# Performance work log

Measured on AMD Instinct MI355X. Metric: run time of the kernel, lower is better.

The kernel has to match this reference:

```python
import jax, jax.numpy as jnp
import numpy as np

B, CI, CO = 2, 32, 32
NX, NY, NZ = 64, 64, 64
M1, M2, M3 = 8, 8, 8
ZH = NZ // 2 + 1


def _dft_mat(N, sign):
    # Dense DFT twiddle matrix W[k, n] = exp(sign * 2j*pi*k*n/N), complex64.
    a = jnp.arange(N)
    ph = (sign * 2.0) * jnp.pi * jnp.outer(a, a).astype(jnp.float32) / N
    return jnp.exp(1j * ph)


def setup_inputs() -> dict:
    key = jax.random.key(0)
    ks = jax.random.split(key, 9)
    scale = 1.0 / (CI * CO)
    x = jax.random.normal(ks[0], (B, CI, NX, NY, NZ), dtype=jnp.float32)
    wshape = (CI, CO, M1, M2, M3)
    names = ['w1r', 'w1i', 'w2r', 'w2i', 'w3r', 'w3i', 'w4r', 'w4i']
    out = {'x': x}
    for i, nm in enumerate(names):
        out[nm] = scale * jax.random.uniform(ks[i + 1], wshape, dtype=jnp.float32)
    return out


def _dht3(x):
    # Naive O(N^2)-per-axis 3D DFT via dense matmuls; return real part.
    Wx = _dft_mat(NX, -1)
    Wy = _dft_mat(NY, -1)
    Wz = _dft_mat(NZ, -1)
    y = x.astype(jnp.complex64)
    y = jnp.einsum('bcxyz,xa->bcayz', y, Wx)
    y = jnp.einsum('bcxyz,ya->bcxaz', y, Wy)
    y = jnp.einsum('bcxyz,za->bcxya', y, Wz)
    return y.real


def _idht3(X):
    # Inverse DFT via dense matmuls; rectangular (ZH -> NZ) on last axis.
    Wxi = _dft_mat(NX, +1) / NX
    Wyi = _dft_mat(NY, +1) / NY
    kz = jnp.arange(ZH)
    nz = jnp.arange(NZ)
    Wzi = jnp.exp(1j * (2.0 * jnp.pi * jnp.outer(kz, nz).astype(jnp.float32) / NZ)) / NZ
    y = jnp.einsum('bcxyz,xa->bcayz', X, Wxi)
    y = jnp.einsum('bcxyz,ya->bcxaz', y, Wyi)
    y = jnp.einsum('bcxyz,za->bcxya', y, Wzi)
    return y.real


def _mul(a, b):
    # compl_mul3d: contract over input channels in the mode block.
    return jnp.einsum('bixyz,ioxyz->boxyz', a, b)


def reference(x, w1r, w1i, w2r, w2i, w3r, w3i, w4r, w4i):
    w1 = w1r + 1j * w1i
    w2 = w2r + 1j * w2i
    w3 = w3r + 1j * w3i
    w4 = w4r + 1j * w4i

    xd = _dht3(x)  # [B, CI, NX, NY, NZ] real

    out = jnp.zeros((B, CO, NX, NY, ZH), dtype=jnp.complex64)
    out = out.at[:, :, :M1, :M2, :M3].set(_mul(xd[:, :, :M1, :M2, :M3], w1))
    out = out.at[:, :, NX - M1:, :M2, :M3].set(_mul(xd[:, :, NX - M1:, :M2, :M3], w2))
    out = out.at[:, :, :M1, NY - M2:, :M3].set(_mul(xd[:, :, :M1, NY - M2:, :M3], w3))
    out = out.at[:, :, NX - M1:, NY - M2:, :M3].set(_mul(xd[:, :, NX - M1:, NY - M2:, :M3], w4))

    return _idht3(out)  # [B, CO, NX, NY, NZ] real
```

## Files before the change

### kernel.cpp

```cpp
#include <hip/hip_runtime.h>

#define PI2_64 0.098174770424681038f


__global__ __launch_bounds__(256) void k_fwd_z(const float* __restrict__ x,
                                               float* __restrict__ z1) {
  __shared__ __align__(16) float lx[256 * 65];
  __shared__ float czs[64], szs[64];
  int tid = threadIdx.x;
  long base = (long)blockIdx.x * (256 * 64);
  const float4* xg = (const float4*)(x + base);
#pragma unroll
  for (int j = 0; j < 16; ++j) {
    int idx = j * 256 + tid;
    float4 v = xg[idx];
    int flat = idx << 2;
    int r = flat >> 6, c = flat & 63;
    float* dst = &lx[r * 65 + c];
    dst[0] = v.x; dst[1] = v.y; dst[2] = v.z; dst[3] = v.w;
  }
  if (tid < 64) {
    float s, c;
    __sincosf(-PI2_64 * (float)tid, &s, &c);
    czs[tid] = c; szs[tid] = s;
  }
  __syncthreads();

  float ar[8] = {0,0,0,0,0,0,0,0}, ai[8] = {0,0,0,0,0,0,0,0};
  const float* row = &lx[tid * 65];
  for (int z = 0; z < 64; ++z) {
    float xv = row[z];
    float bc = czs[z], bs = szs[z];
    float wr = 1.f, wi = 0.f;
#pragma unroll
    for (int k = 0; k < 8; ++k) {
      ar[k] = fmaf(xv, wr, ar[k]);
      ai[k] = fmaf(xv, wi, ai[k]);
      float nr = wr * bc - wi * bs;
      wi = wr * bs + wi * bc;
      wr = nr;
    }
  }
  float4* o = (float4*)(z1 + ((long)blockIdx.x * 256 + tid) * 16);
  o[0] = make_float4(ar[0], ai[0], ar[1], ai[1]);
  o[1] = make_float4(ar[2], ai[2], ar[3], ai[3]);
  o[2] = make_float4(ar[4], ai[4], ar[5], ai[5]);
  o[3] = make_float4(ar[6], ai[6], ar[7], ai[7]);
}

__global__ __launch_bounds__(128) void k_fwd_y(const float* __restrict__ z1,
                                               float* __restrict__ z2) {
  __shared__ __align__(16) float s[64 * 16];
  int tid = threadIdx.x;
  const float4* src = (const float4*)(z1 + (long)blockIdx.x * 1024);
  float4* l4 = (float4*)s;
  l4[tid] = src[tid];
  l4[tid + 128] = src[tid + 128];
  __syncthreads();
  int ky = tid >> 3, kz = tid & 7;
  int f = (ky < 8) ? ky : 48 + ky;
  float bs, bc; __sincosf(-PI2_64 * (float)f, &bs, &bc);
  float wr = 1.f, wi = 0.f, accr = 0.f, acci = 0.f;
  for (int y = 0; y < 64; ++y) {
    float zr = s[y * 16 + kz * 2], zi = s[y * 16 + kz * 2 + 1];
    accr += zr * wr - zi * wi;
    acci += zr * wi + zi * wr;
    float nr = wr * bc - wi * bs;
    wi = wr * bs + wi * bc;
    wr = nr;
  }
  float2* o = (float2*)(z2 + (long)blockIdx.x * 256);
  o[tid] = make_float2(accr, acci);
}

__global__ __launch_bounds__(128) void k_fwd_x(const float* __restrict__ z2,
                                               float* __restrict__ xc) {
  __shared__ __align__(16) float s[64 * 16];
  int tid = threadIdx.x;
  int bi = blockIdx.x >> 4;
  int u = blockIdx.x & 15;
  const float* src = z2 + (long)bi * 16384 + u * 16;
  {
    int xr = tid >> 1, c0 = (tid & 1) * 8;
    const float4* p = (const float4*)(src + xr * 256 + c0);
    float4* q = (float4*)(s + xr * 16 + c0);
    q[0] = p[0]; q[1] = p[1];
  }
  __syncthreads();
  int t = tid >> 3, v = tid & 7;
  int f = (t < 8) ? t : 48 + t;
  float bs, bc; __sincosf(-PI2_64 * (float)f, &bs, &bc);
  float wr = 1.f, wi = 0.f, acc = 0.f;
  for (int xx = 0; xx < 64; ++xx) {
    float zr = s[xx * 16 + v * 2], zi = s[xx * 16 + v * 2 + 1];
    acc += zr * wr - zi * wi;
    float nr = wr * bc - wi * bs;
    wi = wr * bs + wi * bc;
    wr = nr;
  }
  xc[(long)bi * 2048 + t * 128 + u * 8 + v] = acc;
}

__global__ __launch_bounds__(256) void k_mix(const float* __restrict__ xc,
    const float* __restrict__ w1r, const float* __restrict__ w1i,
    const float* __restrict__ w2r, const float* __restrict__ w2i,
    const float* __restrict__ w3r, const float* __restrict__ w3i,
    const float* __restrict__ w4r, const float* __restrict__ w4i,
    float* __restrict__ outm) {
  __shared__ float sx[256];
  int tid = threadIdx.x;
  int b = blockIdx.x >> 8;
  int t = (blockIdx.x >> 4) & 15;
  int u = blockIdx.x & 15;
  {
    int i = tid >> 3, v = tid & 7;
    sx[tid] = xc[(long)(b * 32 + i) * 2048 + t * 128 + u * 8 + v];
  }
  __syncthreads();
  const float* wr_ = (t < 8) ? ((u < 8) ? w1r : w3r) : ((u < 8) ? w2r : w4r);
  const float* wi_ = (t < 8) ? ((u < 8) ? w1i : w3i) : ((u < 8) ? w2i : w4i);
  int tm = t & 7, um = u & 7;
  int o = tid >> 3, v = tid & 7;
  long woff = (long)o * 512 + tm * 64 + um * 8 + v;
  float ar = 0.f, ai = 0.f;
#pragma unroll 4
  for (int i = 0; i < 32; ++i) {
    float xv = sx[i * 8 + v];
    ar = fmaf(xv, wr_[woff + (long)i * 16384], ar);
    ai = fmaf(xv, wi_[woff + (long)i * 16384], ai);
  }
  long oi = (long)(b * 32 + o) * 2048 + t * 128 + u * 8 + v;
  ((float2*)outm)[oi] = make_float2(ar, ai);
}

__global__ __launch_bounds__(512) void k_inv_x(const float* __restrict__ outm,
                                               float* __restrict__ y1) {
  __shared__ float s[256];
  int tid = threadIdx.x;
  int bo = blockIdx.x >> 4;
  int u = blockIdx.x & 15;
  if (tid < 256) {
    int t = tid >> 4, c = tid & 15;
    s[tid] = outm[(long)bo * 4096 + t * 256 + u * 16 + c];
  }
  __syncthreads();
  int xx = tid >> 3, v = tid & 7;
  float bs, bc; __sincosf(PI2_64 * (float)xx, &bs, &bc);
  float wr = 1.f, wi = 0.f, ar = 0.f, ai = 0.f;
#pragma unroll
  for (int t = 0; t < 8; ++t) {
    float pr = s[t * 16 + v * 2], pi = s[t * 16 + v * 2 + 1];
    ar += pr * wr - pi * wi;
    ai += pr * wi + pi * wr;
    float nr = wr * bc - wi * bs; wi = wr * bs + wi * bc; wr = nr;
  }
  wi = -wi;
#pragma unroll
  for (int t = 8; t < 16; ++t) {
    float pr = s[t * 16 + v * 2], pi = s[t * 16 + v * 2 + 1];
    ar += pr * wr - pi * wi;
    ai += pr * wi + pi * wr;
    float nr = wr * bc - wi * bs; wi = wr * bs + wi * bc; wr = nr;
  }
  ((float2*)y1)[(long)bo * 8192 + xx * 128 + u * 8 + v] = make_float2(ar, ai);
}

__global__ __launch_bounds__(512) void k_inv_y(const float* __restrict__ y1,
                                               float* __restrict__ y2) {
  __shared__ float s[256];
  int tid = threadIdx.x;
  if (tid < 256) s[tid] = y1[(long)blockIdx.x * 256 + tid];
  __syncthreads();
  int yy = tid >> 3, v = tid & 7;
  float bs, bc; __sincosf(PI2_64 * (float)yy, &bs, &bc);
  float wr = 1.f, wi = 0.f, ar = 0.f, ai = 0.f;
#pragma unroll
  for (int u = 0; u < 8; ++u) {
    float pr = s[u * 16 + v * 2], pi = s[u * 16 + v * 2 + 1];
    ar += pr * wr - pi * wi;
    ai += pr * wi + pi * wr;
    float nr = wr * bc - wi * bs; wi = wr * bs + wi * bc; wr = nr;
  }
  wi = -wi;
#pragma unroll
  for (int u = 8; u < 16; ++u) {
    float pr = s[u * 16 + v * 2], pi = s[u * 16 + v * 2 + 1];
    ar += pr * wr - pi * wi;
    ai += pr * wi + pi * wr;
    float nr = wr * bc - wi * bs; wi = wr * bs + wi * bc; wr = nr;
  }
  ((float2*)y2)[(long)blockIdx.x * 512 + yy * 8 + v] = make_float2(ar, ai);
}

__global__ __launch_bounds__(256) void k_inv_z(const float* __restrict__ y2,
                                               float* __restrict__ out) {
  __shared__ __align__(16) float s[64 * 16];
  int tid = threadIdx.x;
  const float4* p4 = (const float4*)(y2 + (long)blockIdx.x * 1024);
  float4* l4 = (float4*)s;
  l4[tid] = p4[tid];
  __syncthreads();
  int z = tid & 63, y0 = tid >> 6;
  float bs, bc; __sincosf(PI2_64 * (float)z, &bs, &bc);
  float* o = out + (long)blockIdx.x * 4096;
  const float scale = 1.f / 262144.f;
  for (int yy = 0; yy < 16; ++yy) {
    int y = yy * 4 + y0;
    float wr = 1.f, wi = 0.f, acc = 0.f;
#pragma unroll
    for (int v = 0; v < 8; ++v) {
      float yr = s[y * 16 + v * 2], yi = s[y * 16 + v * 2 + 1];
      acc += yr * wr - yi * wi;
      float nr = wr * bc - wi * bs; wi = wr * bs + wi * bc; wr = nr;
    }
    o[y * 64 + z] = acc * scale;
  }
}

extern "C" void kernel_launch(void* const* d_in, const int* in_sizes, int n_in,
                              void* d_out, int out_size, void* d_ws, size_t ws_size,
                              hipStream_t stream) {
  (void)in_sizes; (void)n_in; (void)out_size; (void)ws_size;
  const float* x   = (const float*)d_in[0];
  const float* w1r = (const float*)d_in[1];
  const float* w1i = (const float*)d_in[2];
  const float* w2r = (const float*)d_in[3];
  const float* w2i = (const float*)d_in[4];
  const float* w3r = (const float*)d_in[5];
  const float* w3i = (const float*)d_in[6];
  const float* w4r = (const float*)d_in[7];
  const float* w4i = (const float*)d_in[8];
  float* out = (float*)d_out;
  float* ws = (float*)d_ws;

  float* z1   = ws;
  float* z2   = ws + 4194304;
  float* xc   = ws + 5242880;
  float* outm = ws + 5373952;
  float* y1   = z2;
  float* y2   = z1;

  k_fwd_z<<<dim3(1024), dim3(256), 0, stream>>>(x, z1);
  k_fwd_y<<<dim3(4096), dim3(128), 0, stream>>>(z1, z2);
  k_fwd_x<<<dim3(1024), dim3(128), 0, stream>>>(z2, xc);
  k_mix<<<dim3(512), dim3(256), 0, stream>>>(xc, w1r, w1i, w2r, w2i,
                                             w3r, w3i, w4r, w4i, outm);
  k_inv_x<<<dim3(1024), dim3(512), 0, stream>>>(outm, y1);
  k_inv_y<<<dim3(4096), dim3(512), 0, stream>>>(y1, y2);
  k_inv_z<<<dim3(4096), dim3(256), 0, stream>>>(y2, out);
}
```

Before: 226.7 us.

## Fuse forward z/y DFT stages and all inverse stages into single kernels

```diff
diff --git a/kernel.cpp b/kernel.cpp
--- a/kernel.cpp
+++ b/kernel.cpp
@@ -3,74 +3,70 @@
 #define PI2_64 0.098174770424681038f
 
 
-__global__ __launch_bounds__(256) void k_fwd_z(const float* __restrict__ x,
-                                               float* __restrict__ z1) {
-  __shared__ __align__(16) float lx[256 * 65];
-  __shared__ float czs[64], szs[64];
-  int tid = threadIdx.x;
-  long base = (long)blockIdx.x * (256 * 64);
-  const float4* xg = (const float4*)(x + base);
-#pragma unroll
-  for (int j = 0; j < 16; ++j) {
+__global__ __launch_bounds__(256) void k_fwd_zy(const float* __restrict__ x,
+                                                float* __restrict__ z2) {
+  __shared__ __align__(16) float sp[64 * 65];
+  __shared__ __align__(8) float2 Z[64 * 9];
+  __shared__ float rc[64], rs[64];
+  int tid = threadIdx.x;
+
+  const float4* xg = (const float4*)(x + (long)blockIdx.x * 4096);
+#pragma unroll
+  for (int j = 0; j < 4; ++j) {
     int idx = j * 256 + tid;
     float4 v = xg[idx];
     int flat = idx << 2;
-    int r = flat >> 6, c = flat & 63;
-    float* dst = &lx[r * 65 + c];
-    dst[0] = v.x; dst[1] = v.y; dst[2] = v.z; dst[3] = v.w;
+    int y = flat >> 6, z = flat & 63;
+    float* d = &sp[y * 65 + z];
+    d[0] = v.x; d[1] = v.y; d[2] = v.z; d[3] = v.w;
   }
   if (tid < 64) {
-    float s, c;
-    __sincosf(-PI2_64 * (float)tid, &s, &c);
-    czs[tid] = c; szs[tid] = s;
-  }
-  __syncthreads();
-
-  float ar[8] = {0,0,0,0,0,0,0,0}, ai[8] = {0,0,0,0,0,0,0,0};
-  const float* row = &lx[tid * 65];
-  for (int z = 0; z < 64; ++z) {
-    float xv = row[z];
-    float bc = czs[z], bs = szs[z];
-    float wr = 1.f, wi = 0.f;
-#pragma unroll
-    for (int k = 0; k < 8; ++k) {
-      ar[k] = fmaf(xv, wr, ar[k]);
-      ai[k] = fmaf(xv, wi, ai[k]);
-      float nr = wr * bc - wi * bs;
-      wi = wr * bs + wi * bc;
-      wr = nr;
-    }
-  }
-  float4* o = (float4*)(z1 + ((long)blockIdx.x * 256 + tid) * 16);
-  o[0] = make_float4(ar[0], ai[0], ar[1], ai[1]);
-  o[1] = make_float4(ar[2], ai[2], ar[3], ai[3]);
-  o[2] = make_float4(ar[4], ai[4], ar[5], ai[5]);
-  o[3] = make_float4(ar[6], ai[6], ar[7], ai[7]);
-}
-
-__global__ __launch_bounds__(128) void k_fwd_y(const float* __restrict__ z1,
-                                               float* __restrict__ z2) {
-  __shared__ __align__(16) float s[64 * 16];
-  int tid = threadIdx.x;
-  const float4* src = (const float4*)(z1 + (long)blockIdx.x * 1024);
-  float4* l4 = (float4*)s;
-  l4[tid] = src[tid];
-  l4[tid + 128] = src[tid + 128];
-  __syncthreads();
-  int ky = tid >> 3, kz = tid & 7;
-  int f = (ky < 8) ? ky : 48 + ky;
-  float bs, bc; __sincosf(-PI2_64 * (float)f, &bs, &bc);
-  float wr = 1.f, wi = 0.f, accr = 0.f, acci = 0.f;
-  for (int y = 0; y < 64; ++y) {
-    float zr = s[y * 16 + kz * 2], zi = s[y * 16 + kz * 2 + 1];
-    accr += zr * wr - zi * wi;
-    acci += zr * wi + zi * wr;
-    float nr = wr * bc - wi * bs;
-    wi = wr * bs + wi * bc;
-    wr = nr;
-  }
-  float2* o = (float2*)(z2 + (long)blockIdx.x * 256);
-  o[tid] = make_float2(accr, acci);
+    float s, c; __sincosf(PI2_64 * (float)tid, &s, &c);
+    rc[tid] = c; rs[tid] = s;
+  }
+  __syncthreads();
+
+  {
+    int y2 = tid >> 3, kz = tid & 7;
+    const float* r0 = &sp[y2 * 65];
+    const float* r1 = &sp[(y2 + 32) * 65];
+    float a0r = 0, a0i = 0, a1r = 0, a1i = 0;
+    int m = 0;
+#pragma unroll 4
+    for (int z = 0; z < 64; ++z) {
+      float c = rc[m], s = rs[m];
+      float x0 = r0[z], x1 = r1[z];
+      a0r = fmaf(x0, c, a0r); a0i = fmaf(-x0, s, a0i);
+      a1r = fmaf(x1, c, a1r); a1i = fmaf(-x1, s, a1i);
+      m = (m + kz) & 63;
+    }
+    Z[y2 * 9 + kz] = make_float2(a0r, a0i);
+    Z[(y2 + 32) * 9 + kz] = make_float2(a1r, a1i);
+  }
+  __syncthreads();
+
+  float2* pb = (float2*)sp;
+  {
+    int kz = tid & 7, ky = (tid >> 3) & 15, h = tid >> 7;
+    int f = (ky < 8) ? ky : (48 + ky);
+    float ar = 0, ai = 0;
+    int m = (h * 32 * f) & 63;
+#pragma unroll 4
+    for (int yy = h * 32; yy < h * 32 + 32; ++yy) {
+      float2 zv = Z[yy * 9 + kz];
+      float c = rc[m], s = rs[m];
+      ar += zv.x * c + zv.y * s;
+      ai += zv.y * c - zv.x * s;
+      m = (m + f) & 63;
+    }
+    pb[ky * 9 + kz + 144 * h] = make_float2(ar, ai);
+  }
+  __syncthreads();
+  if (tid < 128) {
+    int kz = tid & 7, ky = tid >> 3;
+    float2 a = pb[ky * 9 + kz], b = pb[ky * 9 + kz + 144];
+    ((float2*)z2)[(long)blockIdx.x * 128 + tid] = make_float2(a.x + b.x, a.y + b.y);
+  }
 }
 
 __global__ __launch_bounds__(128) void k_fwd_x(const float* __restrict__ z2,
@@ -133,87 +129,97 @@
   ((float2*)outm)[oi] = make_float2(ar, ai);
 }
 
-__global__ __launch_bounds__(512) void k_inv_x(const float* __restrict__ outm,
-                                               float* __restrict__ y1) {
-  __shared__ float s[256];
-  int tid = threadIdx.x;
-  int bo = blockIdx.x >> 4;
-  int u = blockIdx.x & 15;
-  if (tid < 256) {
-    int t = tid >> 4, c = tid & 15;
-    s[tid] = outm[(long)bo * 4096 + t * 256 + u * 16 + c];
-  }
-  __syncthreads();
-  int xx = tid >> 3, v = tid & 7;
-  float bs, bc; __sincosf(PI2_64 * (float)xx, &bs, &bc);
-  float wr = 1.f, wi = 0.f, ar = 0.f, ai = 0.f;
-#pragma unroll
-  for (int t = 0; t < 8; ++t) {
-    float pr = s[t * 16 + v * 2], pi = s[t * 16 + v * 2 + 1];
-    ar += pr * wr - pi * wi;
-    ai += pr * wi + pi * wr;
-    float nr = wr * bc - wi * bs; wi = wr * bs + wi * bc; wr = nr;
-  }
-  wi = -wi;
-#pragma unroll
-  for (int t = 8; t < 16; ++t) {
-    float pr = s[t * 16 + v * 2], pi = s[t * 16 + v * 2 + 1];
-    ar += pr * wr - pi * wi;
-    ai += pr * wi + pi * wr;
-    float nr = wr * bc - wi * bs; wi = wr * bs + wi * bc; wr = nr;
-  }
-  ((float2*)y1)[(long)bo * 8192 + xx * 128 + u * 8 + v] = make_float2(ar, ai);
-}
-
-__global__ __launch_bounds__(512) void k_inv_y(const float* __restrict__ y1,
-                                               float* __restrict__ y2) {
-  __shared__ float s[256];
-  int tid = threadIdx.x;
-  if (tid < 256) s[tid] = y1[(long)blockIdx.x * 256 + tid];
-  __syncthreads();
-  int yy = tid >> 3, v = tid & 7;
-  float bs, bc; __sincosf(PI2_64 * (float)yy, &bs, &bc);
-  float wr = 1.f, wi = 0.f, ar = 0.f, ai = 0.f;
-#pragma unroll
-  for (int u = 0; u < 8; ++u) {
-    float pr = s[u * 16 + v * 2], pi = s[u * 16 + v * 2 + 1];
-    ar += pr * wr - pi * wi;
-    ai += pr * wi + pi * wr;
-    float nr = wr * bc - wi * bs; wi = wr * bs + wi * bc; wr = nr;
-  }
-  wi = -wi;
-#pragma unroll
-  for (int u = 8; u < 16; ++u) {
-    float pr = s[u * 16 + v * 2], pi = s[u * 16 + v * 2 + 1];
-    ar += pr * wr - pi * wi;
-    ai += pr * wi + pi * wr;
-    float nr = wr * bc - wi * bs; wi = wr * bs + wi * bc; wr = nr;
-  }
-  ((float2*)y2)[(long)blockIdx.x * 512 + yy * 8 + v] = make_float2(ar, ai);
-}
-
-__global__ __launch_bounds__(256) void k_inv_z(const float* __restrict__ y2,
-                                               float* __restrict__ out) {
-  __shared__ __align__(16) float s[64 * 16];
-  int tid = threadIdx.x;
-  const float4* p4 = (const float4*)(y2 + (long)blockIdx.x * 1024);
-  float4* l4 = (float4*)s;
-  l4[tid] = p4[tid];
-  __syncthreads();
-  int z = tid & 63, y0 = tid >> 6;
-  float bs, bc; __sincosf(PI2_64 * (float)z, &bs, &bc);
-  float* o = out + (long)blockIdx.x * 4096;
-  const float scale = 1.f / 262144.f;
-  for (int yy = 0; yy < 16; ++yy) {
-    int y = yy * 4 + y0;
-    float wr = 1.f, wi = 0.f, acc = 0.f;
+__global__ __launch_bounds__(256) void k_inv_xyz(const float* __restrict__ outm,
+                                                 float* __restrict__ out) {
+  __shared__ __align__(8) float2 P[16 * 16 * 9];
+  __shared__ __align__(8) float2 Y2[64 * 9];
+  __shared__ __align__(8) float2 Y1[16 * 9];
+  __shared__ float rc[64], rs[64];
+  int tid = threadIdx.x;
+  int bo = blockIdx.x >> 6, xx = blockIdx.x & 63;
+
+  const float2* pg = (const float2*)(outm + (long)bo * 4096);
+#pragma unroll
+  for (int j = 0; j < 8; ++j) {
+    int k = j * 256 + tid;
+    int v = k & 7, tu = k >> 3;
+    P[tu * 9 + v] = pg[k];
+  }
+  if (tid < 64) {
+    float s, c; __sincosf(PI2_64 * (float)tid, &s, &c);
+    rc[tid] = c; rs[tid] = s;
+  }
+  __syncthreads();
+
+  float2* pb = Y2;
+  {
+    int v = tid & 7, u = (tid >> 3) & 15, h = tid >> 7;
+    float ar = 0, ai = 0;
+#pragma unroll
+    for (int t = h * 8; t < h * 8 + 8; ++t) {
+      int f = (t < 8) ? t : (48 + t);
+      int m = (f * xx) & 63;
+      float2 p = P[(t * 16 + u) * 9 + v];
+      float c = rc[m], s = rs[m];
+      ar += p.x * c - p.y * s;
+      ai += p.y * c + p.x * s;
+    }
+    pb[u * 9 + v + 144 * h] = make_float2(ar, ai);
+  }
+  __syncthreads();
+  if (tid < 128) {
+    int v = tid & 7, u = tid >> 3;
+    float2 a = pb[u * 9 + v], b = pb[u * 9 + v + 144];
+    Y1[u * 9 + v] = make_float2(a.x + b.x, a.y + b.y);
+  }
+  __syncthreads();
+
+  {
+    int v = tid & 7, y0 = tid >> 3;
+    int ya = y0, yb = y0 + 32;
+    float ar0 = 0, ai0 = 0, ar1 = 0, ai1 = 0;
+#pragma unroll
+    for (int u = 0; u < 16; ++u) {
+      int f = (u < 8) ? u : (48 + u);
+      float2 q = Y1[u * 9 + v];
+      int ma = (f * ya) & 63, mb = (f * yb) & 63;
+      float ca = rc[ma], sa = rs[ma];
+      float cb = rc[mb], sb = rs[mb];
+      ar0 += q.x * ca - q.y * sa; ai0 += q.y * ca + q.x * sa;
+      ar1 += q.x * cb - q.y * sb; ai1 += q.y * cb + q.x * sb;
+    }
+    __syncthreads();
+    Y2[ya * 9 + v] = make_float2(ar0, ai0);
+    Y2[yb * 9 + v] = make_float2(ar1, ai1);
+  }
+  __syncthreads();
+
+  {
+    int zq = tid & 15, y0 = tid >> 4;
+    int z0 = zq * 4;
+    const float sc = 1.f / 262144.f;
+    float acc[4][4] = {{0,0,0,0},{0,0,0,0},{0,0,0,0},{0,0,0,0}};
 #pragma unroll
     for (int v = 0; v < 8; ++v) {
-      float yr = s[y * 16 + v * 2], yi = s[y * 16 + v * 2 + 1];
-      acc += yr * wr - yi * wi;
-      float nr = wr * bc - wi * bs; wi = wr * bs + wi * bc; wr = nr;
-    }
-    o[y * 64 + z] = acc * scale;
+      int m0 = (v * z0) & 63, m1 = (m0 + v) & 63, m2 = (m1 + v) & 63, m3 = (m2 + v) & 63;
+      float c0 = rc[m0], s0 = rs[m0], c1 = rc[m1], s1 = rs[m1];
+      float c2 = rc[m2], s2 = rs[m2], c3 = rc[m3], s3 = rs[m3];
+#pragma unroll
+      for (int yo = 0; yo < 4; ++yo) {
+        float2 q = Y2[(y0 + yo * 16) * 9 + v];
+        acc[yo][0] += q.x * c0 - q.y * s0;
+        acc[yo][1] += q.x * c1 - q.y * s1;
+        acc[yo][2] += q.x * c2 - q.y * s2;
+        acc[yo][3] += q.x * c3 - q.y * s3;
+      }
+    }
+    float* ob = out + (long)blockIdx.x * 4096;
+#pragma unroll
+    for (int yo = 0; yo < 4; ++yo) {
+      int y = y0 + yo * 16;
+      ((float4*)(ob + y * 64 + z0))[0] =
+          make_float4(acc[yo][0] * sc, acc[yo][1] * sc, acc[yo][2] * sc, acc[yo][3] * sc);
+    }
   }
 }
 
@@ -233,19 +239,13 @@
   float* out = (float*)d_out;
   float* ws = (float*)d_ws;
 
-  float* z1   = ws;
-  float* z2   = ws + 4194304;
-  float* xc   = ws + 5242880;
-  float* outm = ws + 5373952;
-  float* y1   = z2;
-  float* y2   = z1;
-
-  k_fwd_z<<<dim3(1024), dim3(256), 0, stream>>>(x, z1);
-  k_fwd_y<<<dim3(4096), dim3(128), 0, stream>>>(z1, z2);
-  k_fwd_x<<<dim3(1024), dim3(128), 0, stream>>>(z2, xc);
-  k_mix<<<dim3(512), dim3(256), 0, stream>>>(xc, w1r, w1i, w2r, w2i,
-                                             w3r, w3i, w4r, w4i, outm);
-  k_inv_x<<<dim3(1024), dim3(512), 0, stream>>>(outm, y1);
-  k_inv_y<<<dim3(4096), dim3(512), 0, stream>>>(y1, y2);
-  k_inv_z<<<dim3(4096), dim3(256), 0, stream>>>(y2, out);
-}
+  float* z2   = ws;
+  float* xc   = ws + 1048576;
+  float* outm = ws + 1179648;
+
+  k_fwd_zy <<<dim3(4096), dim3(256), 0, stream>>>(x, z2);
+  k_fwd_x  <<<dim3(1024), dim3(128), 0, stream>>>(z2, xc);
+  k_mix    <<<dim3(512),  dim3(256), 0, stream>>>(xc, w1r, w1i, w2r, w2i,
+                                                  w3r, w3i, w4r, w4i, outm);
+  k_inv_xyz<<<dim3(4096), dim3(256), 0, stream>>>(outm, out);
+}
```

Result: faster. 184.2 us (-18.7%).
